# Performance work log

Measured on AMD Instinct MI355X. Metric: run time of the kernel, lower is better.

Reference implementation:

```python
import jax, jax.numpy as jnp
import numpy as np

E = 1024   # embedding_dim
H = 16     # heads
W = 1024   # lag / seq length
B = 4      # batch
D = E // H # head dim


def setup_inputs() -> dict:
    key = jax.random.key(0)
    ks = jax.random.split(key, 5)
    scale = E ** -0.5
    return {
        "x":   jax.random.normal(ks[0], (3, B, E, W), dtype=jnp.float32),
        "L_Q": jax.random.normal(ks[1], (E, E), dtype=jnp.float32) * scale,
        "L_K": jax.random.normal(ks[2], (E, E), dtype=jnp.float32) * scale,
        "L_V": jax.random.normal(ks[3], (E, E), dtype=jnp.float32) * scale,
        "M":   jax.random.normal(ks[4], (E, E), dtype=jnp.float32) * (1.0 / (2 * E)) ** 0.5,
        "b":   jnp.zeros((E, 1), dtype=jnp.float32),
    }


def reference(x, L_Q, L_K, L_V, M, b):
    # x: [3, B, E, W] channels-first; x[0]=K input, x[1]=Q input, x[2]=V input
    K = jnp.einsum('ef,bfw->bew', L_K, x[0])
    Q = jnp.einsum('ef,bfw->bew', L_Q, x[1])
    V = jnp.einsum('ef,bfw->bew', L_V, x[2])
    # reshape to [B, H, D, W]
    Kv = K.reshape(B, H, D, W)
    Qv = Q.reshape(B, H, D, W)
    Vv = V.reshape(B, H, D, W)
    # scores[b,h,q,k] = Q_v^T @ K_v
    scores = jnp.einsum('bhdq,bhdk->bhqk', Qv, Kv)
    # causal mask: -inf for q > k (strictly lower triangle), added BEFORE softmax
    q_idx = jnp.arange(W)[:, None]
    k_idx = jnp.arange(W)[None, :]
    mask = jnp.where(q_idx > k_idx, -jnp.inf, 0.0).astype(scores.dtype)
    scores = scores + mask
    # NON-STANDARD: softmax over the QUERY axis (dim=-2), then scale
    attn = jax.nn.softmax(scores, axis=-2) / (E ** 0.5)
    # V_v @ scores: [B,H,D,W] @ [B,H,W,W] -> [B,H,D,W]
    out = jnp.einsum('bhdq,bhqk->bhdk', Vv, attn).reshape(B, E, W)
    # dense: M @ out + b (dropout identity at inference)
    return jnp.einsum('oe,bew->bow', M, out) + b
```

## Files before the change

kernel.cpp:

```cpp
#include <hip/hip_runtime.h>
#include <stdint.h>
#include <math.h>

#define E_DIM 1024
#define W_DIM 1024
#define EW 1048576L

typedef _Float16 h16;
typedef __attribute__((ext_vector_type(8))) _Float16 h8;
typedef __attribute__((ext_vector_type(4))) float f4;

__device__ __forceinline__ void async_copy16(h16* lds, const h16* g) {
    __builtin_amdgcn_global_load_lds(
        (const __attribute__((address_space(1))) void*)g,
        (__attribute__((address_space(3))) void*)lds, 16, 0, 0);
}

__global__ __launch_bounds__(256) void prep(
    const float* __restrict__ x, const float* __restrict__ LK,
    const float* __restrict__ LQ, const float* __restrict__ LV,
    const float* __restrict__ Mw, h16* __restrict__ xt, h16* __restrict__ wh)
{
    __shared__ float Ts[64][65];
    const int z = blockIdx.z;
    const int t = threadIdx.x;
    if (z < 12) {
        const float* src = x + (long)z * EW;
        h16* dst = xt + (long)z * EW;
        const int e0 = blockIdx.y * 64, w0 = blockIdx.x * 64;
        const int r = t >> 4, c4 = (t & 15) * 4;
        #pragma unroll
        for (int p = 0; p < 4; ++p) {
            float4 v = *reinterpret_cast<const float4*>(src + (long)(e0 + r + p * 16) * W_DIM + w0 + c4);
            Ts[c4 + 0][r + p * 16] = v.x;
            Ts[c4 + 1][r + p * 16] = v.y;
            Ts[c4 + 2][r + p * 16] = v.z;
            Ts[c4 + 3][r + p * 16] = v.w;
        }
        __syncthreads();
        #pragma unroll
        for (int p = 0; p < 4; ++p) {
            int wr = r + p * 16;
            union { h16 h[4]; uint2 u; } o;
            o.h[0] = (h16)Ts[wr][c4 + 0];
            o.h[1] = (h16)Ts[wr][c4 + 1];
            o.h[2] = (h16)Ts[wr][c4 + 2];
            o.h[3] = (h16)Ts[wr][c4 + 3];
            *reinterpret_cast<uint2*>(dst + (long)(w0 + wr) * E_DIM + e0 + c4) = o.u;
        }
    } else {
        const float* srcs[4] = {LK, LQ, LV, Mw};
        const float* s = srcs[z - 12];
        h16* o = wh + (long)(z - 12) * EW;
        long base = ((long)(blockIdx.y * 16 + blockIdx.x)) * 1024 + t;
        #pragma unroll
        for (int k = 0; k < 4; ++k) {
            long i = base + k * 256;
            float4 v = reinterpret_cast<const float4*>(s)[i];
            union { h16 h[4]; uint2 u; } u;
            u.h[0] = (h16)v.x; u.h[1] = (h16)v.y; u.h[2] = (h16)v.z; u.h[3] = (h16)v.w;
            reinterpret_cast<uint2*>(o)[i] = u.u;
        }
    }
}

__global__ __launch_bounds__(256) void gemm_proj3(
    const h16* __restrict__ xh, const h16* __restrict__ Wts,
    h16* __restrict__ KQV)
{
    __shared__ h16 As[128 * 64];
    __shared__ h16 Bs[128 * 64];

    const int t = threadIdx.x;
    const int wave = t >> 6, lane = t & 63;
    const int quad = lane >> 4, l16 = lane & 15;
    const int m0 = blockIdx.y * 128, n0 = blockIdx.x * 128;
    const int wm = (wave >> 1) * 64, wn = (wave & 1) * 64;

    const int proj = blockIdx.z >> 2, bz = blockIdx.z & 3;
    const h16 *A, *Bt; h16* C;
    if (proj == 0)      { A = xh + bz * EW;       Bt = Wts;          C = KQV + bz * EW; }
    else if (proj == 1) { A = xh + (4 + bz) * EW; Bt = Wts + EW;     C = KQV + (4 + bz) * EW; }
    else                { A = Wts + 2 * EW;       Bt = xh + (8 + bz) * EW; C = KQV + (8 + bz) * EW; }

    f4 acc[4][4] = {};

    for (int k0 = 0; k0 < 1024; k0 += 64) {
        __syncthreads();
        #pragma unroll
        for (int j = 0; j < 4; ++j) {
            int g = j * 256 + t, row = g >> 3, cg = (g & 7) ^ (row & 7);
            async_copy16(&As[g * 8], A  + (long)(m0 + row) * E_DIM + k0 + cg * 8);
            async_copy16(&Bs[g * 8], Bt + (long)(n0 + row) * E_DIM + k0 + cg * 8);
        }
        __syncthreads();

        h8 av[4][2], bv[4][2];
        #pragma unroll
        for (int i = 0; i < 4; ++i) {
            int ra = wm + i * 16 + l16, rb = wn + i * 16 + l16;
            #pragma unroll
            for (int c = 0; c < 2; ++c) {
                av[i][c] = *reinterpret_cast<const h8*>(&As[(ra * 8 + ((c * 4 + quad) ^ (l16 & 7))) * 8]);
                bv[i][c] = *reinterpret_cast<const h8*>(&Bs[(rb * 8 + ((c * 4 + quad) ^ (l16 & 7))) * 8]);
            }
        }
        #pragma unroll
        for (int c = 0; c < 2; ++c)
            #pragma unroll
            for (int mt = 0; mt < 4; ++mt)
                #pragma unroll
                for (int nt = 0; nt < 4; ++nt)
                    acc[mt][nt] = __builtin_amdgcn_mfma_f32_16x16x32_f16(av[mt][c], bv[nt][c], acc[mt][nt], 0, 0, 0);
    }

    #pragma unroll
    for (int mt = 0; mt < 4; ++mt)
        #pragma unroll
        for (int i = 0; i < 4; ++i) {
            int m = m0 + wm + mt * 16 + quad * 4 + i;
            #pragma unroll
            for (int nt = 0; nt < 4; ++nt)
                C[(long)m * W_DIM + n0 + wn + nt * 16 + l16] = (h16)acc[mt][nt][i];
        }
}

__global__ __launch_bounds__(256) void gemm_out(
    const h16* __restrict__ A, const h16* __restrict__ Bt,
    float* __restrict__ C, const float* __restrict__ bias)
{
    __shared__ h16 As[64 * 64];
    __shared__ h16 Bs[128 * 64];

    const int t = threadIdx.x;
    const int wave = t >> 6, lane = t & 63;
    const int quad = lane >> 4, l16 = lane & 15;
    const int m0 = blockIdx.y * 64, n0 = blockIdx.x * 128;
    const int wm = (wave >> 1) * 32, wn = (wave & 1) * 64;

    f4 acc[2][4] = {};

    for (int k0 = 0; k0 < 1024; k0 += 64) {
        __syncthreads();
        #pragma unroll
        for (int j = 0; j < 2; ++j) {
            int g = j * 256 + t, row = g >> 3, cg = (g & 7) ^ (row & 7);
            async_copy16(&As[g * 8], A + (long)(m0 + row) * E_DIM + k0 + cg * 8);
        }
        #pragma unroll
        for (int j = 0; j < 4; ++j) {
            int g = j * 256 + t, row = g >> 3, cg = (g & 7) ^ (row & 7);
            async_copy16(&Bs[g * 8], Bt + (long)(n0 + row) * E_DIM + k0 + cg * 8);
        }
        __syncthreads();

        h8 av[2][2], bv[4][2];
        #pragma unroll
        for (int c = 0; c < 2; ++c) {
            #pragma unroll
            for (int mt = 0; mt < 2; ++mt) {
                int r = wm + mt * 16 + l16;
                av[mt][c] = *reinterpret_cast<const h8*>(&As[(r * 8 + ((c * 4 + quad) ^ (l16 & 7))) * 8]);
            }
            #pragma unroll
            for (int nt = 0; nt < 4; ++nt) {
                int r = wn + nt * 16 + l16;
                bv[nt][c] = *reinterpret_cast<const h8*>(&Bs[(r * 8 + ((c * 4 + quad) ^ (l16 & 7))) * 8]);
            }
        }
        #pragma unroll
        for (int c = 0; c < 2; ++c)
            #pragma unroll
            for (int mt = 0; mt < 2; ++mt)
                #pragma unroll
                for (int nt = 0; nt < 4; ++nt)
                    acc[mt][nt] = __builtin_amdgcn_mfma_f32_16x16x32_f16(av[mt][c], bv[nt][c], acc[mt][nt], 0, 0, 0);
    }

    #pragma unroll
    for (int mt = 0; mt < 2; ++mt)
        #pragma unroll
        for (int i = 0; i < 4; ++i) {
            int m = m0 + wm + mt * 16 + quad * 4 + i;
            float bv_ = bias ? bias[m] : 0.f;
            #pragma unroll
            for (int nt = 0; nt < 4; ++nt) {
                int n = n0 + wn + nt * 16 + l16;
                C[(long)(n >> 10) * EW + (long)m * W_DIM + (n & 1023)] = acc[mt][nt][i] + bv_;
            }
        }
}

__global__ __launch_bounds__(256) void attn_mfma(
    const h16* __restrict__ Kt, const h16* __restrict__ Qt,
    const h16* __restrict__ V, h16* __restrict__ AoT)
{
    __shared__ h16 Qs[2][64 * 64];
    __shared__ h16 Vs[2][64 * 64];
    __shared__ h16 Ps[4][32 * 64];

    const int t = threadIdx.x, wave = t >> 6, lane = t & 63;
    const int quad = lane >> 4, l16 = lane & 15;
    const int y = blockIdx.y;
    const int b = y >> 4, h = y & 15;
    const int cxor = (y & 7) ^ (((y >> 5) & 1) ? 7 : 0);
    const int ktb = (int)blockIdx.x ^ cxor;
    const int nit = 2 * ktb + 2;
    const int kwave = ktb * 128 + wave * 32;
    const int kc0 = kwave + l16, kc1 = kc0 + 16;

    const h16* Ktb_ = Kt + (long)b * EW + h * 64;
    const h16* Qtb  = Qt + (long)b * EW + h * 64;
    const h16* Vb   = V  + (long)b * EW + (long)(h * 64) * W_DIM;
    h16* Pw = &Ps[wave][0];

    h8 kb00 = *reinterpret_cast<const h8*>(Ktb_ + (long)kc0 * E_DIM + quad * 8);
    h8 kb01 = *reinterpret_cast<const h8*>(Ktb_ + (long)kc0 * E_DIM + 32 + quad * 8);
    h8 kb10 = *reinterpret_cast<const h8*>(Ktb_ + (long)kc1 * E_DIM + quad * 8);
    h8 kb11 = *reinterpret_cast<const h8*>(Ktb_ + (long)kc1 * E_DIM + 32 + quad * 8);

    #pragma unroll
    for (int j = 0; j < 2; ++j) {
        int g = j * 256 + t, row = g >> 3, cg = (g & 7) ^ (row & 7);
        async_copy16(&Qs[0][g * 8], Qtb + (long)row * E_DIM + cg * 8);
        async_copy16(&Vs[0][g * 8], Vb + (long)row * W_DIM + cg * 8);
    }

    const float L2E = 1.442695041f;
    float mr0 = -1e30f, mr1 = -1e30f, ls0 = 0.f, ls1 = 0.f;
    f4 O[4][2] = {};

    for (int it = 0; it < nit; ++it) {
        const int q0 = it * 64;
        __syncthreads();
        if (it + 1 < nit) {
            const int nb = (it + 1) & 1, q1 = q0 + 64;
            #pragma unroll
            for (int j = 0; j < 2; ++j) {
                int g = j * 256 + t, row = g >> 3, cg = (g & 7) ^ (row & 7);
                async_copy16(&Qs[nb][g * 8], Qtb + (long)(q1 + row) * E_DIM + cg * 8);
                async_copy16(&Vs[nb][g * 8], Vb + (long)row * W_DIM + q1 + cg * 8);
            }
        }
        if (q0 > kwave + 31) continue;

        const h16* qs = Qs[it & 1];
        const h16* vs = Vs[it & 1];

        f4 S0[4], S1[4];
        __builtin_amdgcn_s_setprio(1);
        #pragma unroll
        for (int nt = 0; nt < 4; ++nt) {
            int row = nt * 16 + l16;
            h8 a0 = *reinterpret_cast<const h8*>(&qs[(row * 8 + (quad ^ (l16 & 7))) * 8]);
            h8 a1 = *reinterpret_cast<const h8*>(&qs[(row * 8 + ((4 + quad) ^ (l16 & 7))) * 8]);
            f4 s0 = {}, s1 = {};
            s0 = __builtin_amdgcn_mfma_f32_16x16x32_f16(a0, kb00, s0, 0, 0, 0);
            s1 = __builtin_amdgcn_mfma_f32_16x16x32_f16(a0, kb10, s1, 0, 0, 0);
            s0 = __builtin_amdgcn_mfma_f32_16x16x32_f16(a1, kb01, s0, 0, 0, 0);
            s1 = __builtin_amdgcn_mfma_f32_16x16x32_f16(a1, kb11, s1, 0, 0, 0);
            S0[nt] = s0; S1[nt] = s1;
        }
        __builtin_amdgcn_s_setprio(0);

        if (it >= 2 * ktb) {
            #pragma unroll
            for (int nt = 0; nt < 4; ++nt)
                #pragma unroll
                for (int i = 0; i < 4; ++i) {
                    int q = q0 + nt * 16 + quad * 4 + i;
                    if (q > kc0) S0[nt][i] = -1e30f;
                    if (q > kc1) S1[nt][i] = -1e30f;
                }
        }

        float mx0 = -1e30f, mx1 = -1e30f;
        #pragma unroll
        for (int nt = 0; nt < 4; ++nt) {
            float t0 = fmaxf(fmaxf(S0[nt][0], S0[nt][1]), fmaxf(S0[nt][2], S0[nt][3]));
            float t1 = fmaxf(fmaxf(S1[nt][0], S1[nt][1]), fmaxf(S1[nt][2], S1[nt][3]));
            mx0 = fmaxf(mx0, t0); mx1 = fmaxf(mx1, t1);
        }
        mx0 = fmaxf(mx0, __shfl_xor(mx0, 16)); mx1 = fmaxf(mx1, __shfl_xor(mx1, 16));
        mx0 = fmaxf(mx0, __shfl_xor(mx0, 32)); mx1 = fmaxf(mx1, __shfl_xor(mx1, 32));

        if (__any((mx0 - mr0 > 8.f) || (mx1 - mr1 > 8.f))) {
            float nm0 = fmaxf(mr0, mx0), nm1 = fmaxf(mr1, mx1);
            float al0 = exp2f((mr0 - nm0) * L2E), al1 = exp2f((mr1 - nm1) * L2E);
            mr0 = nm0; mr1 = nm1;
            ls0 *= al0; ls1 *= al1;
            #pragma unroll
            for (int dt = 0; dt < 4; ++dt)
                #pragma unroll
                for (int i = 0; i < 4; ++i) { O[dt][0][i] *= al0; O[dt][1][i] *= al1; }
        }

        const float mc0 = mr0 * L2E, mc1 = mr1 * L2E;
        float tsa = 0.f, tsb = 0.f, tsc = 0.f, tsd = 0.f;
        #pragma unroll
        for (int nt = 0; nt < 4; ++nt)
            #pragma unroll
            for (int i = 0; i < 4; ++i) {
                float p0 = exp2f(fmaf(S0[nt][i], L2E, -mc0));
                float p1 = exp2f(fmaf(S1[nt][i], L2E, -mc1));
                S0[nt][i] = p0; S1[nt][i] = p1;
                if (i & 1) { tsb += p0; tsd += p1; } else { tsa += p0; tsc += p1; }
            }
        float ts0 = tsa + tsb, ts1 = tsc + tsd;
        ts0 += __shfl_xor(ts0, 16); ts1 += __shfl_xor(ts1, 16);
        ts0 += __shfl_xor(ts0, 32); ts1 += __shfl_xor(ts1, 32);
        ls0 += ts0; ls1 += ts1;

        #pragma unroll
        for (int nt = 0; nt < 4; ++nt) {
            int sg = ((nt * 2 + (quad >> 1)) ^ (l16 & 7)) * 8 + (quad & 1) * 4;
            union { h16 hh[4]; uint2 u2; } u0, u1;
            #pragma unroll
            for (int i = 0; i < 4; ++i) { u0.hh[i] = (h16)S0[nt][i]; u1.hh[i] = (h16)S1[nt][i]; }
            *reinterpret_cast<uint2*>(Pw + l16 * 64 + sg) = u0.u2;
            *reinterpret_cast<uint2*>(Pw + (16 + l16) * 64 + sg) = u1.u2;
        }
        asm volatile("" ::: "memory");

        __builtin_amdgcn_s_setprio(1);
        #pragma unroll
        for (int c = 0; c < 2; ++c) {
            int sg = ((c * 4 + quad) ^ (l16 & 7)) * 8;
            h8 p0 = *reinterpret_cast<const h8*>(Pw + l16 * 64 + sg);
            h8 p1 = *reinterpret_cast<const h8*>(Pw + (16 + l16) * 64 + sg);
            #pragma unroll
            for (int dt = 0; dt < 4; ++dt) {
                int r = dt * 16 + l16;
                h8 va = *reinterpret_cast<const h8*>(&vs[(r * 8 + ((c * 4 + quad) ^ (l16 & 7))) * 8]);
                O[dt][0] = __builtin_amdgcn_mfma_f32_16x16x32_f16(va, p0, O[dt][0], 0, 0, 0);
                O[dt][1] = __builtin_amdgcn_mfma_f32_16x16x32_f16(va, p1, O[dt][1], 0, 0, 0);
            }
        }
        __builtin_amdgcn_s_setprio(0);
    }

    const float inv0 = 0.03125f / ls0, inv1 = 0.03125f / ls1;
    #pragma unroll
    for (int dt = 0; dt < 4; ++dt) {
        int sg = ((dt * 2 + (quad >> 1)) ^ (l16 & 7)) * 8 + (quad & 1) * 4;
        union { h16 hh[4]; uint2 u2; } u0, u1;
        #pragma unroll
        for (int i = 0; i < 4; ++i) {
            u0.hh[i] = (h16)(O[dt][0][i] * inv0);
            u1.hh[i] = (h16)(O[dt][1][i] * inv1);
        }
        *reinterpret_cast<uint2*>(Pw + l16 * 64 + sg) = u0.u2;
        *reinterpret_cast<uint2*>(Pw + (16 + l16) * 64 + sg) = u1.u2;
    }
    asm volatile("" ::: "memory");
    #pragma unroll
    for (int g = 0; g < 2; ++g)
        #pragma unroll
        for (int j = 0; j < 2; ++j) {
            int sg = ((quad * 2 + j) ^ (l16 & 7)) * 8;
            uint4 vv = *reinterpret_cast<const uint4*>(Pw + (g * 16 + l16) * 64 + sg);
            *reinterpret_cast<uint4*>(AoT + (long)b * EW
                                      + (long)(kwave + g * 16 + l16) * E_DIM
                                      + h * 64 + quad * 16 + j * 8) = vv;
        }
}

extern "C" void kernel_launch(void* const* d_in, const int* in_sizes, int n_in,
                              void* d_out, int out_size, void* d_ws, size_t ws_size,
                              hipStream_t stream)
{
    const float* x  = (const float*)d_in[0];
    const float* LQ = (const float*)d_in[1];
    const float* LK = (const float*)d_in[2];
    const float* LV = (const float*)d_in[3];
    const float* Mw = (const float*)d_in[4];
    const float* bb = (const float*)d_in[5];
    float* out = (float*)d_out;
    h16* ws = (h16*)d_ws;

    h16* xh  = ws;
    h16* LKh = ws + 12 * EW;
    h16* Mh  = ws + 15 * EW;
    h16* Kp  = ws + 16 * EW;
    h16* Qp  = ws + 20 * EW;
    h16* Vp  = ws + 24 * EW;
    h16* Ao  = ws + 28 * EW;

    dim3 blk(256);
    prep<<<dim3(16, 16, 16), blk, 0, stream>>>(x, LK, LQ, LV, Mw, xh, LKh);
    gemm_proj3<<<dim3(8, 8, 12), blk, 0, stream>>>(xh, LKh, Kp);
    attn_mfma<<<dim3(8, 64), blk, 0, stream>>>(Kp, Qp, Vp, Ao);
    gemm_out<<<dim3(32, 16), blk, 0, stream>>>(Mh, Ao, out, bb);
}
```

Measured before the change: 201.3 us.

## Load Q and V directly from global into registers per wave, dropping LDS staging

The attention kernel stops staging Q and V tiles in double-buffered shared memory with async copies and block-wide barriers. Each wave now loads its Q and V fragments straight from global memory into registers and runs its own per-wave trip count, so waves with less causal work can finish early. The block-to-tile mapping also changes from an XOR swizzle to a reversed order, so the heaviest tiles launch first. In exchange it loses cross-wave reuse through LDS, adds redundant global/L2 traffic (each wave reloads the same tiles), raises register pressure, and exposes load latency without software prefetch.

```diff
diff --git a/kernel.cpp b/kernel.cpp
--- a/kernel.cpp
+++ b/kernel.cpp
@@ -195,19 +195,16 @@
     const h16* __restrict__ Kt, const h16* __restrict__ Qt,
     const h16* __restrict__ V, h16* __restrict__ AoT)
 {
-    __shared__ h16 Qs[2][64 * 64];
-    __shared__ h16 Vs[2][64 * 64];
     __shared__ h16 Ps[4][32 * 64];
 
     const int t = threadIdx.x, wave = t >> 6, lane = t & 63;
     const int quad = lane >> 4, l16 = lane & 15;
     const int y = blockIdx.y;
     const int b = y >> 4, h = y & 15;
-    const int cxor = (y & 7) ^ (((y >> 5) & 1) ? 7 : 0);
-    const int ktb = (int)blockIdx.x ^ cxor;
-    const int nit = 2 * ktb + 2;
+    const int ktb = 7 - (int)blockIdx.x;
     const int kwave = ktb * 128 + wave * 32;
     const int kc0 = kwave + l16, kc1 = kc0 + 16;
+    const int nitw = 2 * ktb + 1 + (wave >> 1);
 
     const h16* Ktb_ = Kt + (long)b * EW + h * 64;
     const h16* Qtb  = Qt + (long)b * EW + h * 64;
@@ -219,46 +216,37 @@
     h8 kb10 = *reinterpret_cast<const h8*>(Ktb_ + (long)kc1 * E_DIM + quad * 8);
     h8 kb11 = *reinterpret_cast<const h8*>(Ktb_ + (long)kc1 * E_DIM + 32 + quad * 8);
 
-    #pragma unroll
-    for (int j = 0; j < 2; ++j) {
-        int g = j * 256 + t, row = g >> 3, cg = (g & 7) ^ (row & 7);
-        async_copy16(&Qs[0][g * 8], Qtb + (long)row * E_DIM + cg * 8);
-        async_copy16(&Vs[0][g * 8], Vb + (long)row * W_DIM + cg * 8);
-    }
-
     const float L2E = 1.442695041f;
     float mr0 = -1e30f, mr1 = -1e30f, ls0 = 0.f, ls1 = 0.f;
     f4 O[4][2] = {};
 
-    for (int it = 0; it < nit; ++it) {
+    for (int it = 0; it < nitw; ++it) {
         const int q0 = it * 64;
-        __syncthreads();
-        if (it + 1 < nit) {
-            const int nb = (it + 1) & 1, q1 = q0 + 64;
-            #pragma unroll
-            for (int j = 0; j < 2; ++j) {
-                int g = j * 256 + t, row = g >> 3, cg = (g & 7) ^ (row & 7);
-                async_copy16(&Qs[nb][g * 8], Qtb + (long)(q1 + row) * E_DIM + cg * 8);
-                async_copy16(&Vs[nb][g * 8], Vb + (long)row * W_DIM + q1 + cg * 8);
-            }
-        }
-        if (q0 > kwave + 31) continue;
-
-        const h16* qs = Qs[it & 1];
-        const h16* vs = Vs[it & 1];
+
+        h8 qa[4][2];
+        #pragma unroll
+        for (int nt = 0; nt < 4; ++nt)
+            #pragma unroll
+            for (int c = 0; c < 2; ++c)
+                qa[nt][c] = *reinterpret_cast<const h8*>(
+                    Qtb + (long)(q0 + nt * 16 + l16) * E_DIM + c * 32 + quad * 8);
+        h8 va[4][2];
+        #pragma unroll
+        for (int dt = 0; dt < 4; ++dt)
+            #pragma unroll
+            for (int c = 0; c < 2; ++c)
+                va[dt][c] = *reinterpret_cast<const h8*>(
+                    Vb + (long)(dt * 16 + l16) * W_DIM + q0 + c * 32 + quad * 8);
 
         f4 S0[4], S1[4];
         __builtin_amdgcn_s_setprio(1);
         #pragma unroll
         for (int nt = 0; nt < 4; ++nt) {
-            int row = nt * 16 + l16;
-            h8 a0 = *reinterpret_cast<const h8*>(&qs[(row * 8 + (quad ^ (l16 & 7))) * 8]);
-            h8 a1 = *reinterpret_cast<const h8*>(&qs[(row * 8 + ((4 + quad) ^ (l16 & 7))) * 8]);
             f4 s0 = {}, s1 = {};
-            s0 = __builtin_amdgcn_mfma_f32_16x16x32_f16(a0, kb00, s0, 0, 0, 0);
-            s1 = __builtin_amdgcn_mfma_f32_16x16x32_f16(a0, kb10, s1, 0, 0, 0);
-            s0 = __builtin_amdgcn_mfma_f32_16x16x32_f16(a1, kb01, s0, 0, 0, 0);
-            s1 = __builtin_amdgcn_mfma_f32_16x16x32_f16(a1, kb11, s1, 0, 0, 0);
+            s0 = __builtin_amdgcn_mfma_f32_16x16x32_f16(qa[nt][0], kb00, s0, 0, 0, 0);
+            s1 = __builtin_amdgcn_mfma_f32_16x16x32_f16(qa[nt][0], kb10, s1, 0, 0, 0);
+            s0 = __builtin_amdgcn_mfma_f32_16x16x32_f16(qa[nt][1], kb01, s0, 0, 0, 0);
+            s1 = __builtin_amdgcn_mfma_f32_16x16x32_f16(qa[nt][1], kb11, s1, 0, 0, 0);
             S0[nt] = s0; S1[nt] = s1;
         }
         __builtin_amdgcn_s_setprio(0);
@@ -330,10 +318,8 @@
             h8 p1 = *reinterpret_cast<const h8*>(Pw + (16 + l16) * 64 + sg);
             #pragma unroll
             for (int dt = 0; dt < 4; ++dt) {
-                int r = dt * 16 + l16;
-                h8 va = *reinterpret_cast<const h8*>(&vs[(r * 8 + ((c * 4 + quad) ^ (l16 & 7))) * 8]);
-                O[dt][0] = __builtin_amdgcn_mfma_f32_16x16x32_f16(va, p0, O[dt][0], 0, 0, 0);
-                O[dt][1] = __builtin_amdgcn_mfma_f32_16x16x32_f16(va, p1, O[dt][1], 0, 0, 0);
+                O[dt][0] = __builtin_amdgcn_mfma_f32_16x16x32_f16(va[dt][c], p0, O[dt][0], 0, 0, 0);
+                O[dt][1] = __builtin_amdgcn_mfma_f32_16x16x32_f16(va[dt][c], p1, O[dt][1], 0, 0, 0);
             }
         }
         __builtin_amdgcn_s_setprio(0);
```

New measurement: 223.0 us. 1.11x slower.

## Double-buffer GEMM LDS tiles and software-pipeline attention PV with next QK

Applied to the files above, without the earlier changes.

Both projection and output GEMMs now use two LDS buffers, prefetching the next K-tile before computing the current one and dropping one barrier per iteration. The attention kernel is software-pipelined: V fragments are held in registers, and the P·V MFMAs for the previous tile are issued after the QK MFMAs of the current tile so matrix work overlaps softmax. This adds LDS and register pressure, which may lower occupancy, and needs careful handling of the P buffer reuse across iterations.

```diff
diff --git a/kernel.cpp b/kernel.cpp
--- a/kernel.cpp
+++ b/kernel.cpp
@@ -68,8 +68,8 @@
     const h16* __restrict__ xh, const h16* __restrict__ Wts,
     h16* __restrict__ KQV)
 {
-    __shared__ h16 As[128 * 64];
-    __shared__ h16 Bs[128 * 64];
+    __shared__ h16 As[2][128 * 64];
+    __shared__ h16 Bs[2][128 * 64];
 
     const int t = threadIdx.x;
     const int wave = t >> 6, lane = t & 63;
@@ -85,24 +85,35 @@
 
     f4 acc[4][4] = {};
 
-    for (int k0 = 0; k0 < 1024; k0 += 64) {
+    #pragma unroll
+    for (int j = 0; j < 4; ++j) {
+        int g = j * 256 + t, row = g >> 3, cg = (g & 7) ^ (row & 7);
+        async_copy16(&As[0][g * 8], A  + (long)(m0 + row) * E_DIM + cg * 8);
+        async_copy16(&Bs[0][g * 8], Bt + (long)(n0 + row) * E_DIM + cg * 8);
+    }
+
+    for (int i = 0; i < 16; ++i) {
         __syncthreads();
-        #pragma unroll
-        for (int j = 0; j < 4; ++j) {
-            int g = j * 256 + t, row = g >> 3, cg = (g & 7) ^ (row & 7);
-            async_copy16(&As[g * 8], A  + (long)(m0 + row) * E_DIM + k0 + cg * 8);
-            async_copy16(&Bs[g * 8], Bt + (long)(n0 + row) * E_DIM + k0 + cg * 8);
-        }
-        __syncthreads();
+        if (i + 1 < 16) {
+            const int k1 = (i + 1) * 64, nb = (i + 1) & 1;
+            #pragma unroll
+            for (int j = 0; j < 4; ++j) {
+                int g = j * 256 + t, row = g >> 3, cg = (g & 7) ^ (row & 7);
+                async_copy16(&As[nb][g * 8], A  + (long)(m0 + row) * E_DIM + k1 + cg * 8);
+                async_copy16(&Bs[nb][g * 8], Bt + (long)(n0 + row) * E_DIM + k1 + cg * 8);
+            }
+        }
+        const h16* as = As[i & 1];
+        const h16* bs = Bs[i & 1];
 
         h8 av[4][2], bv[4][2];
         #pragma unroll
-        for (int i = 0; i < 4; ++i) {
-            int ra = wm + i * 16 + l16, rb = wn + i * 16 + l16;
+        for (int ii = 0; ii < 4; ++ii) {
+            int ra = wm + ii * 16 + l16, rb = wn + ii * 16 + l16;
             #pragma unroll
             for (int c = 0; c < 2; ++c) {
-                av[i][c] = *reinterpret_cast<const h8*>(&As[(ra * 8 + ((c * 4 + quad) ^ (l16 & 7))) * 8]);
-                bv[i][c] = *reinterpret_cast<const h8*>(&Bs[(rb * 8 + ((c * 4 + quad) ^ (l16 & 7))) * 8]);
+                av[ii][c] = *reinterpret_cast<const h8*>(&as[(ra * 8 + ((c * 4 + quad) ^ (l16 & 7))) * 8]);
+                bv[ii][c] = *reinterpret_cast<const h8*>(&bs[(rb * 8 + ((c * 4 + quad) ^ (l16 & 7))) * 8]);
             }
         }
         #pragma unroll
@@ -129,8 +140,8 @@
     const h16* __restrict__ A, const h16* __restrict__ Bt,
     float* __restrict__ C, const float* __restrict__ bias)
 {
-    __shared__ h16 As[64 * 64];
-    __shared__ h16 Bs[128 * 64];
+    __shared__ h16 As[2][64 * 64];
+    __shared__ h16 Bs[2][128 * 64];
 
     const int t = threadIdx.x;
     const int wave = t >> 6, lane = t & 63;
@@ -140,19 +151,34 @@
 
     f4 acc[2][4] = {};
 
-    for (int k0 = 0; k0 < 1024; k0 += 64) {
+    #pragma unroll
+    for (int j = 0; j < 2; ++j) {
+        int g = j * 256 + t, row = g >> 3, cg = (g & 7) ^ (row & 7);
+        async_copy16(&As[0][g * 8], A + (long)(m0 + row) * E_DIM + cg * 8);
+    }
+    #pragma unroll
+    for (int j = 0; j < 4; ++j) {
+        int g = j * 256 + t, row = g >> 3, cg = (g & 7) ^ (row & 7);
+        async_copy16(&Bs[0][g * 8], Bt + (long)(n0 + row) * E_DIM + cg * 8);
+    }
+
+    for (int i = 0; i < 16; ++i) {
         __syncthreads();
-        #pragma unroll
-        for (int j = 0; j < 2; ++j) {
-            int g = j * 256 + t, row = g >> 3, cg = (g & 7) ^ (row & 7);
-            async_copy16(&As[g * 8], A + (long)(m0 + row) * E_DIM + k0 + cg * 8);
-        }
-        #pragma unroll
-        for (int j = 0; j < 4; ++j) {
-            int g = j * 256 + t, row = g >> 3, cg = (g & 7) ^ (row & 7);
-            async_copy16(&Bs[g * 8], Bt + (long)(n0 + row) * E_DIM + k0 + cg * 8);
-        }
-        __syncthreads();
+        if (i + 1 < 16) {
+            const int k1 = (i + 1) * 64, nb = (i + 1) & 1;
+            #pragma unroll
+            for (int j = 0; j < 2; ++j) {
+                int g = j * 256 + t, row = g >> 3, cg = (g & 7) ^ (row & 7);
+                async_copy16(&As[nb][g * 8], A + (long)(m0 + row) * E_DIM + k1 + cg * 8);
+            }
+            #pragma unroll
+            for (int j = 0; j < 4; ++j) {
+                int g = j * 256 + t, row = g >> 3, cg = (g & 7) ^ (row & 7);
+                async_copy16(&Bs[nb][g * 8], Bt + (long)(n0 + row) * E_DIM + k1 + cg * 8);
+            }
+        }
+        const h16* as = As[i & 1];
+        const h16* bs = Bs[i & 1];
 
         h8 av[2][2], bv[4][2];
         #pragma unroll
@@ -160,12 +186,12 @@
             #pragma unroll
             for (int mt = 0; mt < 2; ++mt) {
                 int r = wm + mt * 16 + l16;
-                av[mt][c] = *reinterpret_cast<const h8*>(&As[(r * 8 + ((c * 4 + quad) ^ (l16 & 7))) * 8]);
+                av[mt][c] = *reinterpret_cast<const h8*>(&as[(r * 8 + ((c * 4 + quad) ^ (l16 & 7))) * 8]);
             }
             #pragma unroll
             for (int nt = 0; nt < 4; ++nt) {
                 int r = wn + nt * 16 + l16;
-                bv[nt][c] = *reinterpret_cast<const h8*>(&Bs[(r * 8 + ((c * 4 + quad) ^ (l16 & 7))) * 8]);
+                bv[nt][c] = *reinterpret_cast<const h8*>(&bs[(r * 8 + ((c * 4 + quad) ^ (l16 & 7))) * 8]);
             }
         }
         #pragma unroll
@@ -208,6 +234,7 @@
     const int nit = 2 * ktb + 2;
     const int kwave = ktb * 128 + wave * 32;
     const int kc0 = kwave + l16, kc1 = kc0 + 16;
+    const int nitw = ((kwave + 31) >> 6) + 1;
 
     const h16* Ktb_ = Kt + (long)b * EW + h * 64;
     const h16* Qtb  = Qt + (long)b * EW + h * 64;
@@ -229,6 +256,7 @@
     const float L2E = 1.442695041f;
     float mr0 = -1e30f, mr1 = -1e30f, ls0 = 0.f, ls1 = 0.f;
     f4 O[4][2] = {};
+    h8 vap[4][2];
 
     for (int it = 0; it < nit; ++it) {
         const int q0 = it * 64;
@@ -242,87 +270,121 @@
                 async_copy16(&Vs[nb][g * 8], Vb + (long)row * W_DIM + q1 + cg * 8);
             }
         }
-        if (q0 > kwave + 31) continue;
-
+        const bool act = it < nitw;
         const h16* qs = Qs[it & 1];
         const h16* vs = Vs[it & 1];
 
         f4 S0[4], S1[4];
-        __builtin_amdgcn_s_setprio(1);
-        #pragma unroll
-        for (int nt = 0; nt < 4; ++nt) {
-            int row = nt * 16 + l16;
-            h8 a0 = *reinterpret_cast<const h8*>(&qs[(row * 8 + (quad ^ (l16 & 7))) * 8]);
-            h8 a1 = *reinterpret_cast<const h8*>(&qs[(row * 8 + ((4 + quad) ^ (l16 & 7))) * 8]);
-            f4 s0 = {}, s1 = {};
-            s0 = __builtin_amdgcn_mfma_f32_16x16x32_f16(a0, kb00, s0, 0, 0, 0);
-            s1 = __builtin_amdgcn_mfma_f32_16x16x32_f16(a0, kb10, s1, 0, 0, 0);
-            s0 = __builtin_amdgcn_mfma_f32_16x16x32_f16(a1, kb01, s0, 0, 0, 0);
-            s1 = __builtin_amdgcn_mfma_f32_16x16x32_f16(a1, kb11, s1, 0, 0, 0);
-            S0[nt] = s0; S1[nt] = s1;
-        }
-        __builtin_amdgcn_s_setprio(0);
-
-        if (it >= 2 * ktb) {
+        h8 va[4][2];
+        if (act) {
+            #pragma unroll
+            for (int dt = 0; dt < 4; ++dt)
+                #pragma unroll
+                for (int c = 0; c < 2; ++c) {
+                    int r = dt * 16 + l16;
+                    va[dt][c] = *reinterpret_cast<const h8*>(&vs[(r * 8 + ((c * 4 + quad) ^ (l16 & 7))) * 8]);
+                }
+            __builtin_amdgcn_s_setprio(1);
+            #pragma unroll
+            for (int nt = 0; nt < 4; ++nt) {
+                int row = nt * 16 + l16;
+                h8 a0 = *reinterpret_cast<const h8*>(&qs[(row * 8 + (quad ^ (l16 & 7))) * 8]);
+                h8 a1 = *reinterpret_cast<const h8*>(&qs[(row * 8 + ((4 + quad) ^ (l16 & 7))) * 8]);
+                f4 s0 = {}, s1 = {};
+                s0 = __builtin_amdgcn_mfma_f32_16x16x32_f16(a0, kb00, s0, 0, 0, 0);
+                s1 = __builtin_amdgcn_mfma_f32_16x16x32_f16(a0, kb10, s1, 0, 0, 0);
+                s0 = __builtin_amdgcn_mfma_f32_16x16x32_f16(a1, kb01, s0, 0, 0, 0);
+                s1 = __builtin_amdgcn_mfma_f32_16x16x32_f16(a1, kb11, s1, 0, 0, 0);
+                S0[nt] = s0; S1[nt] = s1;
+            }
+            __builtin_amdgcn_s_setprio(0);
+        }
+
+        if (it > 0 && it - 1 < nitw) {
+            __builtin_amdgcn_s_setprio(1);
+            #pragma unroll
+            for (int c = 0; c < 2; ++c) {
+                int sg = ((c * 4 + quad) ^ (l16 & 7)) * 8;
+                h8 p0 = *reinterpret_cast<const h8*>(Pw + l16 * 64 + sg);
+                h8 p1 = *reinterpret_cast<const h8*>(Pw + (16 + l16) * 64 + sg);
+                #pragma unroll
+                for (int dt = 0; dt < 4; ++dt) {
+                    O[dt][0] = __builtin_amdgcn_mfma_f32_16x16x32_f16(vap[dt][c], p0, O[dt][0], 0, 0, 0);
+                    O[dt][1] = __builtin_amdgcn_mfma_f32_16x16x32_f16(vap[dt][c], p1, O[dt][1], 0, 0, 0);
+                }
+            }
+            __builtin_amdgcn_s_setprio(0);
+        }
+
+        if (act) {
+            if (it >= 2 * ktb) {
+                #pragma unroll
+                for (int nt = 0; nt < 4; ++nt)
+                    #pragma unroll
+                    for (int i = 0; i < 4; ++i) {
+                        int q = q0 + nt * 16 + quad * 4 + i;
+                        if (q > kc0) S0[nt][i] = -1e30f;
+                        if (q > kc1) S1[nt][i] = -1e30f;
+                    }
+            }
+
+            float mx0 = -1e30f, mx1 = -1e30f;
+            #pragma unroll
+            for (int nt = 0; nt < 4; ++nt) {
+                float t0 = fmaxf(fmaxf(S0[nt][0], S0[nt][1]), fmaxf(S0[nt][2], S0[nt][3]));
+                float t1 = fmaxf(fmaxf(S1[nt][0], S1[nt][1]), fmaxf(S1[nt][2], S1[nt][3]));
+                mx0 = fmaxf(mx0, t0); mx1 = fmaxf(mx1, t1);
+            }
+            mx0 = fmaxf(mx0, __shfl_xor(mx0, 16)); mx1 = fmaxf(mx1, __shfl_xor(mx1, 16));
+            mx0 = fmaxf(mx0, __shfl_xor(mx0, 32)); mx1 = fmaxf(mx1, __shfl_xor(mx1, 32));
+
+            if (__any((mx0 - mr0 > 8.f) || (mx1 - mr1 > 8.f))) {
+                float nm0 = fmaxf(mr0, mx0), nm1 = fmaxf(mr1, mx1);
+                float al0 = exp2f((mr0 - nm0) * L2E), al1 = exp2f((mr1 - nm1) * L2E);
+                mr0 = nm0; mr1 = nm1;
+                ls0 *= al0; ls1 *= al1;
+                #pragma unroll
+                for (int dt = 0; dt < 4; ++dt)
+                    #pragma unroll
+                    for (int i = 0; i < 4; ++i) { O[dt][0][i] *= al0; O[dt][1][i] *= al1; }
+            }
+
+            const float mc0 = mr0 * L2E, mc1 = mr1 * L2E;
+            float tsa = 0.f, tsb = 0.f, tsc = 0.f, tsd = 0.f;
             #pragma unroll
             for (int nt = 0; nt < 4; ++nt)
                 #pragma unroll
                 for (int i = 0; i < 4; ++i) {
-                    int q = q0 + nt * 16 + quad * 4 + i;
-                    if (q > kc0) S0[nt][i] = -1e30f;
-                    if (q > kc1) S1[nt][i] = -1e30f;
+                    float p0 = exp2f(fmaf(S0[nt][i], L2E, -mc0));
+                    float p1 = exp2f(fmaf(S1[nt][i], L2E, -mc1));
+                    S0[nt][i] = p0; S1[nt][i] = p1;
+                    if (i & 1) { tsb += p0; tsd += p1; } else { tsa += p0; tsc += p1; }
                 }
-        }
-
-        float mx0 = -1e30f, mx1 = -1e30f;
-        #pragma unroll
-        for (int nt = 0; nt < 4; ++nt) {
-            float t0 = fmaxf(fmaxf(S0[nt][0], S0[nt][1]), fmaxf(S0[nt][2], S0[nt][3]));
-            float t1 = fmaxf(fmaxf(S1[nt][0], S1[nt][1]), fmaxf(S1[nt][2], S1[nt][3]));
-            mx0 = fmaxf(mx0, t0); mx1 = fmaxf(mx1, t1);
-        }
-        mx0 = fmaxf(mx0, __shfl_xor(mx0, 16)); mx1 = fmaxf(mx1, __shfl_xor(mx1, 16));
-        mx0 = fmaxf(mx0, __shfl_xor(mx0, 32)); mx1 = fmaxf(mx1, __shfl_xor(mx1, 32));
-
-        if (__any((mx0 - mr0 > 8.f) || (mx1 - mr1 > 8.f))) {
-            float nm0 = fmaxf(mr0, mx0), nm1 = fmaxf(mr1, mx1);
-            float al0 = exp2f((mr0 - nm0) * L2E), al1 = exp2f((mr1 - nm1) * L2E);
-            mr0 = nm0; mr1 = nm1;
-            ls0 *= al0; ls1 *= al1;
+            float ts0 = tsa + tsb, ts1 = tsc + tsd;
+            ts0 += __shfl_xor(ts0, 16); ts1 += __shfl_xor(ts1, 16);
+            ts0 += __shfl_xor(ts0, 32); ts1 += __shfl_xor(ts1, 32);
+            ls0 += ts0; ls1 += ts1;
+
+            asm volatile("" ::: "memory");
+            #pragma unroll
+            for (int nt = 0; nt < 4; ++nt) {
+                int sg = ((nt * 2 + (quad >> 1)) ^ (l16 & 7)) * 8 + (quad & 1) * 4;
+                union { h16 hh[4]; uint2 u2; } u0, u1;
+                #pragma unroll
+                for (int i = 0; i < 4; ++i) { u0.hh[i] = (h16)S0[nt][i]; u1.hh[i] = (h16)S1[nt][i]; }
+                *reinterpret_cast<uint2*>(Pw + l16 * 64 + sg) = u0.u2;
+                *reinterpret_cast<uint2*>(Pw + (16 + l16) * 64 + sg) = u1.u2;
+            }
+            asm volatile("" ::: "memory");
+
             #pragma unroll
             for (int dt = 0; dt < 4; ++dt)
                 #pragma unroll
-                for (int i = 0; i < 4; ++i) { O[dt][0][i] *= al0; O[dt][1][i] *= al1; }
-        }
-
-        const float mc0 = mr0 * L2E, mc1 = mr1 * L2E;
-        float tsa = 0.f, tsb = 0.f, tsc = 0.f, tsd = 0.f;
-        #pragma unroll
-        for (int nt = 0; nt < 4; ++nt)
-            #pragma unroll
-            for (int i = 0; i < 4; ++i) {
-                float p0 = exp2f(fmaf(S0[nt][i], L2E, -mc0));
-                float p1 = exp2f(fmaf(S1[nt][i], L2E, -mc1));
-                S0[nt][i] = p0; S1[nt][i] = p1;
-                if (i & 1) { tsb += p0; tsd += p1; } else { tsa += p0; tsc += p1; }
-            }
-        float ts0 = tsa + tsb, ts1 = tsc + tsd;
-        ts0 += __shfl_xor(ts0, 16); ts1 += __shfl_xor(ts1, 16);
-        ts0 += __shfl_xor(ts0, 32); ts1 += __shfl_xor(ts1, 32);
-        ls0 += ts0; ls1 += ts1;
-
-        #pragma unroll
-        for (int nt = 0; nt < 4; ++nt) {
-            int sg = ((nt * 2 + (quad >> 1)) ^ (l16 & 7)) * 8 + (quad & 1) * 4;
-            union { h16 hh[4]; uint2 u2; } u0, u1;
-            #pragma unroll
-            for (int i = 0; i < 4; ++i) { u0.hh[i] = (h16)S0[nt][i]; u1.hh[i] = (h16)S1[nt][i]; }
-            *reinterpret_cast<uint2*>(Pw + l16 * 64 + sg) = u0.u2;
-            *reinterpret_cast<uint2*>(Pw + (16 + l16) * 64 + sg) = u1.u2;
-        }
-        asm volatile("" ::: "memory");
-
-        __builtin_amdgcn_s_setprio(1);
+                for (int c = 0; c < 2; ++c) vap[dt][c] = va[dt][c];
+        }
+    }
+
+    if (nitw == nit) {
         #pragma unroll
         for (int c = 0; c < 2; ++c) {
             int sg = ((c * 4 + quad) ^ (l16 & 7)) * 8;
@@ -330,16 +392,14 @@
             h8 p1 = *reinterpret_cast<const h8*>(Pw + (16 + l16) * 64 + sg);
             #pragma unroll
             for (int dt = 0; dt < 4; ++dt) {
-                int r = dt * 16 + l16;
-                h8 va = *reinterpret_cast<const h8*>(&vs[(r * 8 + ((c * 4 + quad) ^ (l16 & 7))) * 8]);
-                O[dt][0] = __builtin_amdgcn_mfma_f32_16x16x32_f16(va, p0, O[dt][0], 0, 0, 0);
-                O[dt][1] = __builtin_amdgcn_mfma_f32_16x16x32_f16(va, p1, O[dt][1], 0, 0, 0);
-            }
-        }
-        __builtin_amdgcn_s_setprio(0);
+                O[dt][0] = __builtin_amdgcn_mfma_f32_16x16x32_f16(vap[dt][c], p0, O[dt][0], 0, 0, 0);
+                O[dt][1] = __builtin_amdgcn_mfma_f32_16x16x32_f16(vap[dt][c], p1, O[dt][1], 0, 0, 0);
+            }
+        }
     }
 
     const float inv0 = 0.03125f / ls0, inv1 = 0.03125f / ls1;
+    asm volatile("" ::: "memory");
     #pragma unroll
     for (int dt = 0; dt < 4; ++dt) {
         int sg = ((dt * 2 + (quad >> 1)) ^ (l16 & 7)) * 8 + (quad & 1) * 4;
```

Result: slower. 239.3 us (+18.9%).
